# Optimization experiments

Hardware: AMD Instinct MI355X
Metric: run time of the kernel (lower is better)

The kernel has to match this reference:

```python
import jax, jax.numpy as jnp
import numpy as np

POI, EMB, UNITS, QDIM, B = 5000, 256, 512, 256, 64


def setup_inputs() -> dict:
    key = jax.random.key(0)
    ks = jax.random.split(key, 16)
    s = 0.05
    return {
        "x": jax.random.randint(ks[0], (B,), 0, POI),
        "query": jax.random.normal(ks[1], (B, QDIM), jnp.float32),
        "poi_embedding": jax.random.normal(ks[2], (POI, EMB), jnp.float32),
        "A_hat": jax.random.normal(ks[3], (B, B), jnp.float32),
        "dec_hidden": jax.random.normal(ks[4], (B, UNITS), jnp.float32),
        "cat_dec_hidden": jax.random.normal(ks[5], (1, B, UNITS), jnp.float32),
        # GRUCell params (keras order z, r, h; reset_after=True -> bias [2, 3*units])
        "gru_kernel": jax.random.normal(ks[6], (EMB + QDIM, 3 * UNITS), jnp.float32) * s,
        "gru_rec_kernel": jax.random.normal(ks[7], (UNITS, 3 * UNITS), jnp.float32) * s,
        "gru_bias": jax.random.normal(ks[8], (2, 3 * UNITS), jnp.float32) * s,
        # Bahdanau attention params
        "W1_w": jax.random.normal(ks[9], (EMB, UNITS), jnp.float32) * s,
        "W1_b": jnp.zeros((UNITS,), jnp.float32),
        "W2_w": jax.random.normal(ks[10], (UNITS, UNITS), jnp.float32) * s,
        "W2_b": jnp.zeros((UNITS,), jnp.float32),
        "V_w": jax.random.normal(ks[11], (UNITS, 1), jnp.float32) * s,
        "V_b": jnp.zeros((1,), jnp.float32),
        # output dense: concat(context EMB, output_ UNITS, cat_hidden UNITS) -> POI
        "fc_w": jax.random.normal(ks[12], (EMB + 2 * UNITS, POI), jnp.float32) * s,
        "fc_b": jnp.zeros((POI,), jnp.float32),
    }


def _gru_cell(x, h, kernel, rec_kernel, bias):
    # keras GRUCell, reset_after=True, gate order (z, r, h)
    xm = x @ kernel + bias[0]        # [B, 3U]
    hm = h @ rec_kernel + bias[1]    # [B, 3U]
    xz, xr, xh = jnp.split(xm, 3, axis=-1)
    hz, hr, hh = jnp.split(hm, 3, axis=-1)
    z = jax.nn.sigmoid(xz + hz)
    r = jax.nn.sigmoid(xr + hr)
    h_cand = jnp.tanh(xh + r * hh)
    h_new = z * h + (1.0 - z) * h_cand
    return h_new, h_new


def reference(x, query, poi_embedding, A_hat, dec_hidden, cat_dec_hidden,
              gru_kernel, gru_rec_kernel, gru_bias,
              W1_w, W1_b, W2_w, W2_b, V_w, V_b, fc_w, fc_b):
    emb = poi_embedding
    x1 = jnp.concatenate([emb[x], query], axis=1)          # [B, EMB+QDIM]
    output_, state = _gru_cell(x1, dec_hidden, gru_kernel, gru_rec_kernel, gru_bias)
    # Bahdanau attention: values are the full embedding table [POI, EMB]
    v_proj = emb @ W1_w + W1_b                              # [POI, U]
    q_proj = output_ @ W2_w + W2_b                          # [B, U]
    score = jnp.tanh(v_proj[None, :, :] + q_proj[:, None, :]) @ V_w + V_b  # [B, POI, 1]
    attn = jax.nn.softmax(score, axis=1)                    # [B, POI, 1]
    context = jnp.sum(attn * emb[None, :, :], axis=1)       # [B, EMB]
    out_cat = jnp.concatenate([context, output_, cat_dec_hidden[0]], axis=1)
    logits = out_cat @ fc_w + fc_b                          # [B, POI]
    return (logits, state, output_)
```

## Files before the change

### kernel.cpp

```cpp
#include <hip/hip_runtime.h>
#include <hip/hip_bf16.h>

typedef __bf16 bf16;
typedef __bf16 bf16x8 __attribute__((ext_vector_type(8)));
typedef float f32x4 __attribute__((ext_vector_type(4)));

#define BB 64
#define EMB 256
#define UNITS 512
#define POI 5000
#define KCAT 1280
#define SCLD 5024
#define L2E 1.4426950408889634f

__device__ __forceinline__ float rcp_(float x){ return __builtin_amdgcn_rcpf(x); }
__device__ __forceinline__ float exp2_(float x){ return __builtin_amdgcn_exp2f(x); }

__device__ __forceinline__ bf16x8 cvt8(f32x4 a0, f32x4 a1){
  bf16x8 o;
#pragma unroll
  for(int j=0;j<4;j++){ o[j]=(bf16)a0[j]; o[4+j]=(bf16)a1[j]; }
  return o;
}

__device__ __forceinline__ f32x4 mm16r(const float* __restrict__ ap, const float* __restrict__ B,
                                       int ldb, int K, int nc, int lane){
  int q = lane >> 4;
  f32x4 acc = {0.f,0.f,0.f,0.f};
  ap += q*8;
  const float* bp = B + (size_t)(q*8)*ldb + nc;
#pragma unroll 2
  for(int k0 = 0; k0 < K; k0 += 32){
    bf16x8 a = cvt8(*(const f32x4*)ap, *(const f32x4*)(ap+4));
    bf16x8 b;
#pragma unroll
    for(int j=0;j<8;j++) b[j] = (bf16)bp[(size_t)j*ldb];
    acc = __builtin_amdgcn_mfma_f32_16x16x32_bf16(a, b, acc, 0, 0, 0);
    ap += 32; bp += (size_t)32*ldb;
  }
  return acc;
}
__device__ __forceinline__ f32x4 mm16f(const float* __restrict__ A, const float* __restrict__ B,
                                       int lda, int ldb, int K, int mr, int nc, int lane){
  return mm16r(A + (size_t)mr*lda, B, ldb, K, nc, lane);
}

__device__ __forceinline__ void t64(const float* __restrict__ src, int srcLd, int nRv,
    int r0, int c0, int cW, bf16* __restrict__ dstT, int dstLd, int dstRmax,
    int lane, int w){
  int r = r0 + lane;
  bool rv = r < nRv;
  int cw4 = cW >> 2;
  int cb = c0 + w*cw4;
  for(int c8=0;c8<cw4;c8+=8){
    int c = cb + c8;
    f32x4 v0={0.f,0.f,0.f,0.f}, v1={0.f,0.f,0.f,0.f};
    if(rv){ v0 = *(const f32x4*)(src + (size_t)r*srcLd + c);
            v1 = *(const f32x4*)(src + (size_t)r*srcLd + c + 4); }
    if(r < dstRmax){
#pragma unroll
      for(int j=0;j<4;j++){
        dstT[(size_t)(c+j)*dstLd + r]   = (bf16)v0[j];
        dstT[(size_t)(c+4+j)*dstLd + r] = (bf16)v1[j];
      }
    }
  }
}

__global__ __launch_bounds__(256) void k_prep0(
    const float* __restrict__ emb, const float* __restrict__ W1, const float* __restrict__ W2,
    const float* __restrict__ gruK, const float* __restrict__ gruR,
    float* __restrict__ out, float* __restrict__ outc,
    bf16* __restrict__ embB, bf16* __restrict__ embTb,
    bf16* __restrict__ W1Tb, bf16* __restrict__ W2Tb,
    bf16* __restrict__ gruKTb, bf16* __restrict__ gruRTb,
    unsigned* __restrict__ mxb, float* __restrict__ sumb){
  int bx = blockIdx.x, t = threadIdx.x, lane = t & 63, w = t >> 6;
  if(bx < 80){
    int r0 = bx*64;
    for(int ch = t; ch < 2048; ch += 256){
      int r = r0 + (ch >> 5), cc = (ch & 31)*8;
      if(r < POI){
        f32x4 v0 = *(const f32x4*)(emb + (size_t)r*EMB + cc);
        f32x4 v1 = *(const f32x4*)(emb + (size_t)r*EMB + cc + 4);
        *(bf16x8*)(embB + (size_t)r*EMB + cc) = cvt8(v0, v1);
      }
    }
  } else if(bx < 240){
    int i = bx - 80;
    t64(emb, EMB, POI, (i>>1)*64, (i&1)*128, 128, embTb, SCLD, SCLD, lane, w);
  } else if(bx < 256){
    int i = bx - 240;
    t64(W2, UNITS, UNITS, (i>>1)*64, (i&1)*256, 256, W2Tb, UNITS, UNITS, lane, w);
  } else if(bx < 264){
    int i = bx - 256;
    t64(W1, UNITS, EMB, (i>>1)*64, (i&1)*256, 256, W1Tb, EMB, EMB, lane, w);
  } else if(bx < 328){
    int i = bx - 264;
    t64(gruK, 1536, 512, (i>>3)*64, (i&7)*192, 192, gruKTb, 512, 512, lane, w);
  } else if(bx < 392){
    int i = bx - 328;
    t64(gruR, 1536, 512, (i>>3)*64, (i&7)*192, 192, gruRTb, 512, 512, lane, w);
  } else if(bx < 432){
    f32x4 z = {0.f,0.f,0.f,0.f};
    for(int i = (bx-392)*256 + t; i < 80000; i += 40*256) ((f32x4*)out)[i] = z;
  } else if(bx < 434){
    f32x4 z = {0.f,0.f,0.f,0.f};
    for(int i = (bx-432)*256 + t; i < 4096; i += 512){
      int b = i >> 6, jj = i & 63;
      ((f32x4*)(outc + (size_t)b*KCAT))[jj] = z;
    }
  } else {
    if(t < BB){ mxb[t] = 0u; sumb[t] = 0.f; }
  }
}

__global__ __launch_bounds__(256) void k_gru(const int* __restrict__ x, const float* __restrict__ query,
    const bf16* __restrict__ embB, const float* __restrict__ h0,
    const bf16* __restrict__ gruKTb, const bf16* __restrict__ gruRTb,
    float* __restrict__ xmP, float* __restrict__ hmP){
  int lane = threadIdx.x & 63, w = threadIdx.x >> 6;
  int col = blockIdx.x*16 + (lane & 15);
  int y = blockIdx.y, z = blockIdx.z;
  int mr = w*16 + (lane & 15);
  int q = lane >> 4;
  const bf16* bp = (y ? gruRTb : gruKTb) + (size_t)col*512 + z*256 + q*8;
  float* C = (y ? hmP : xmP) + (size_t)z*BB*1536;
  f32x4 acc = {0.f,0.f,0.f,0.f};
  if(y == 0 && z == 0){
    const bf16* ap = embB + (size_t)x[mr]*EMB + q*8;
#pragma unroll
    for(int k0=0;k0<256;k0+=32){
      bf16x8 a = *(const bf16x8*)ap, b = *(const bf16x8*)bp;
      acc = __builtin_amdgcn_mfma_f32_16x16x32_bf16(a,b,acc,0,0,0);
      ap += 32; bp += 32;
    }
  } else {
    const float* apf = y ? (h0 + (size_t)mr*512 + z*256 + q*8)
                         : (query + (size_t)mr*256 + q*8);
#pragma unroll
    for(int k0=0;k0<256;k0+=32){
      bf16x8 a = cvt8(*(const f32x4*)apf, *(const f32x4*)(apf+4));
      bf16x8 b = *(const bf16x8*)bp;
      acc = __builtin_amdgcn_mfma_f32_16x16x32_bf16(a,b,acc,0,0,0);
      apf += 32; bp += 32;
    }
  }
  int rb = w*16 + (lane >> 4)*4;
#pragma unroll
  for(int r=0;r<4;r++) C[(size_t)(rb+r)*1536 + col] = acc[r];
}

__global__ __launch_bounds__(256) void k_gates(const float* __restrict__ xmP, const float* __restrict__ hmP,
                        const float* __restrict__ bias, const float* __restrict__ h0,
                        const float* __restrict__ catd,
                        float* __restrict__ hn, float* __restrict__ outc, float* __restrict__ dout){
  int b = blockIdx.x, u = blockIdx.y*256 + threadIdx.x;
  const float* x0 = xmP + b*1536; const float* x1s = xmP + (size_t)BB*1536 + b*1536;
  const float* h0s = hmP + b*1536; const float* h1s = hmP + (size_t)BB*1536 + b*1536;
  float xz = x0[u]      + x1s[u]      + bias[u];
  float xg = x0[512+u]  + x1s[512+u]  + bias[512+u];
  float xh = x0[1024+u] + x1s[1024+u] + bias[1024+u];
  float hz = h0s[u]      + h1s[u]      + bias[1536+u];
  float hg = h0s[512+u]  + h1s[512+u]  + bias[2048+u];
  float hh = h0s[1024+u] + h1s[1024+u] + bias[2560+u];
  float z = rcp_(1.f + exp2_(-L2E*(xz+hz)));
  float r = rcp_(1.f + exp2_(-L2E*(xg+hg)));
  float ca = xh + r*hh;
  ca = fminf(fmaxf(ca, -15.f), 15.f);
  float e = exp2_(2.f*L2E*ca);
  float hc = (e - 1.f)*rcp_(e + 1.f);
  float h = h0[b*512+u];
  float v = z*h + (1.f - z)*hc;
  hn[b*512+u] = v;
  outc[b*KCAT + 256 + u] = v;
  outc[b*KCAT + 768 + u] = catd[(size_t)b*512 + u];
  dout[(size_t)POI*BB + (size_t)b*512 + u] = v;
  dout[(size_t)POI*BB + (size_t)BB*512 + (size_t)b*512 + u] = v;
}

__global__ __launch_bounds__(256) void k_qproj(const float* __restrict__ hn, const bf16* __restrict__ W2Tb,
                        const float* __restrict__ W2b, float* __restrict__ Eq){
  __shared__ float accs[16][17];
  int t = threadIdx.x, lane = t & 63, w = t >> 6;
  int c16 = blockIdx.x & 31, r16 = blockIdx.x >> 5;
  for(int i=t;i<16*17;i+=256) ((float*)accs)[i] = 0.f;
  __syncthreads();
  int q = lane >> 4;
  int mr  = r16*16 + (lane & 15);
  int col = c16*16 + (lane & 15);
  const float* ap = hn + (size_t)mr*UNITS + w*128 + q*8;
  const bf16*  bp = W2Tb + (size_t)col*UNITS + w*128 + q*8;
  f32x4 acc = {0.f,0.f,0.f,0.f};
#pragma unroll
  for(int k0=0;k0<128;k0+=32){
    bf16x8 a = cvt8(*(const f32x4*)ap, *(const f32x4*)(ap+4));
    bf16x8 b = *(const bf16x8*)bp;
    acc = __builtin_amdgcn_mfma_f32_16x16x32_bf16(a,b,acc,0,0,0);
    ap += 32; bp += 32;
  }
#pragma unroll
  for(int r=0;r<4;r++) atomicAdd(&accs[q*4+r][lane & 15], acc[r]);
  __syncthreads();
  int r = t >> 4, c = t & 15;
  int colg = c16*16 + c;
  float v = (accs[r][c] + W2b[colg])*(2.f*L2E);
  Eq[(size_t)(r16*16+r)*UNITS + colg] = exp2_(fminf(fmaxf(v,-40.f),40.f));
}

template<int NY>
__global__ __launch_bounds__(256, 8) void k_vscore(
    const bf16* __restrict__ embB, const bf16* __restrict__ W1Tb,
    const float* __restrict__ W1b, const float* __restrict__ Eq,
    const float* __restrict__ Vw, float* __restrict__ scS){
  constexpr int USL = 512/NY;
  __shared__ float evsT[USL][20];
  __shared__ float vws[USL];
  int t = threadIdx.x, lane = t & 63, w = t >> 6;
  int p0 = blockIdx.x*16, uh = blockIdx.y*USL;
  int q = lane >> 4;
  int mr = p0 + (lane & 15); if(mr > POI-1) mr = POI-1;
#pragma unroll
  for(int i=0;i<USL/64;i++){
    int colL = (w + 4*i)*16 + (lane & 15);
    const bf16* ap = embB + (size_t)mr*EMB + q*8;
    const bf16* bp = W1Tb + (size_t)(uh+colL)*EMB + q*8;
    f32x4 acc = {0.f,0.f,0.f,0.f};
#pragma unroll
    for(int k0=0;k0<EMB;k0+=32){
      bf16x8 a = *(const bf16x8*)ap, b = *(const bf16x8*)bp;
      acc = __builtin_amdgcn_mfma_f32_16x16x32_bf16(a,b,acc,0,0,0);
      ap += 32; bp += 32;
    }
    float bn = W1b[uh+colL];
    f32x4 ev;
#pragma unroll
    for(int r=0;r<4;r++){
      float v = (acc[r] + bn)*(2.f*L2E);
      ev[r] = exp2_(fminf(fmaxf(v,-40.f),40.f));
    }
    *(f32x4*)&evsT[colL][q*4] = ev;
  }
  if(t < USL) vws[t] = Vw[uh + t];
  __syncthreads();
  int pg = t & 3, b = t >> 2;
  const float* qrow = Eq + (size_t)b*UNITS + uh;
  f32x4 s = {0.f,0.f,0.f,0.f};
#pragma unroll 4
  for(int u4=0; u4<USL/4; ++u4){
    f32x4 q4 = *(const f32x4*)&qrow[u4*4];
    f32x4 wv = *(const f32x4*)&vws[u4*4];
#pragma unroll
    for(int j=0;j<4;j++){
      f32x4 ev = *(const f32x4*)&evsT[u4*4+j][4*pg];
#pragma unroll
      for(int e=0;e<4;e++)
        s[e] += wv[j]*rcp_(ev[e]*q4[j] + 1.f);
    }
  }
  int pA = p0 + 4*pg;
  float* srow = scS + (size_t)blockIdx.y*BB*SCLD + (size_t)b*SCLD + pA;
  if(pA + 3 < POI) *(f32x4*)srow = s;
  else {
#pragma unroll
    for(int e=0;e<4;e++) if(pA+e < POI) srow[e] = s[e];
  }
}

__global__ __launch_bounds__(256) void k_smax_a(float* __restrict__ sc, unsigned* __restrict__ mxb,
                                                int nslab){
  __shared__ float red[256];
  int b = blockIdx.x, y = blockIdx.y, t = threadIdx.x;
  float* sA = sc + (size_t)b*SCLD;
  int pend = (y+1)*640; if(pend > POI) pend = POI;
  float mx = -3.4e38f;
  for(int p = y*640 + t; p < pend; p += 256){
    float acc = sA[p];
    for(int s2=1;s2<nslab;s2++) acc += sA[(size_t)s2*BB*SCLD + p];
    float v = -2.f*acc;
    sA[p] = v;
    mx = fmaxf(mx, v);
  }
  red[t] = mx; __syncthreads();
  for(int o=128;o>0;o>>=1){ if(t<o) red[t]=fmaxf(red[t],red[t+o]); __syncthreads(); }
  if(t==0){
    unsigned u = __float_as_uint(red[0]);
    unsigned key = (u & 0x80000000u) ? ~u : (u | 0x80000000u);
    atomicMax(mxb + b, key);
  }
}

__global__ __launch_bounds__(256) void k_smax_b(float* __restrict__ sc, const unsigned* __restrict__ mxb,
                                                float* __restrict__ sumb){
  __shared__ float red[256];
  int b = blockIdx.x, y = blockIdx.y, t = threadIdx.x;
  unsigned key = mxb[b];
  unsigned uu = (key & 0x80000000u) ? (key ^ 0x80000000u) : ~key;
  float M = __uint_as_float(uu);
  float* sA = sc + (size_t)b*SCLD;
  int pend = (y+1)*640; if(pend > POI) pend = POI;
  float sm = 0.f;
  for(int p = y*640 + t; p < pend; p += 256){
    float e = exp2_((sA[p] - M)*L2E);
    sA[p] = e;
    sm += e;
  }
  if(y == 7 && t < SCLD-POI) sA[POI + t] = 0.f;
  red[t] = sm; __syncthreads();
  for(int o=128;o>0;o>>=1){ if(t<o) red[t]+=red[t+o]; __syncthreads(); }
  if(t==0) atomicAdd(sumb + b, red[0]);
}

__global__ __launch_bounds__(256) void k_ctx(const float* __restrict__ wb, const bf16* __restrict__ embTb,
                                             const float* __restrict__ sumb, float* __restrict__ outc){
  int lane = threadIdx.x & 63, w = threadIdx.x >> 6;
  int n = blockIdx.x*16 + (lane & 15);
  int ky = blockIdx.y;
  int kbeg = ky*64;
  int K = (ky == 78) ? 32 : 64;
  int mr = w*16 + (lane & 15);
  int q = lane >> 4;
  const float* ap = wb + (size_t)mr*SCLD + kbeg + q*8;
  const bf16*  bp = embTb + (size_t)n*SCLD + kbeg + q*8;
  f32x4 acc = {0.f,0.f,0.f,0.f};
  for(int k0=0;k0<K;k0+=32){
    bf16x8 a = cvt8(*(const f32x4*)ap, *(const f32x4*)(ap+4));
    bf16x8 b = *(const bf16x8*)bp;
    acc = __builtin_amdgcn_mfma_f32_16x16x32_bf16(a,b,acc,0,0,0);
    ap += 32; bp += 32;
  }
  int rb = w*16 + (lane >> 4)*4;
#pragma unroll
  for(int r=0;r<4;r++) atomicAdd(&outc[(size_t)(rb+r)*KCAT + n], acc[r]*rcp_(sumb[rb+r]));
}

__global__ __launch_bounds__(256) void k_logits(const float* __restrict__ A, const float* __restrict__ Bw,
                        const float* __restrict__ fcb, float* __restrict__ out){
  int lane = threadIdx.x & 63, w = threadIdx.x >> 6;
  int n = blockIdx.x*16 + (lane & 15);
  int nc = n < POI ? n : POI-1;
  int ky = blockIdx.y, kbeg = ky*160;
  f32x4 acc = mm16f(A + kbeg, Bw + (size_t)kbeg*POI, KCAT, POI, 160,
                    w*16 + (lane & 15), nc, lane);
  int rb = w*16 + (lane >> 4)*4;
  if(n < POI){
    float bn = (ky == 0) ? fcb[n] : 0.f;
#pragma unroll
    for(int r=0;r<4;r++) atomicAdd(&out[(size_t)(rb+r)*POI + n], acc[r] + bn);
  }
}

extern "C" void kernel_launch(void* const* d_in, const int* in_sizes, int n_in,
                              void* d_out, int out_size, void* d_ws, size_t ws_size,
                              hipStream_t stream){
  const int*   x     = (const int*)d_in[0];
  const float* query = (const float*)d_in[1];
  const float* emb   = (const float*)d_in[2];
  const float* h0    = (const float*)d_in[4];
  const float* catd  = (const float*)d_in[5];
  const float* gruK  = (const float*)d_in[6];
  const float* gruR  = (const float*)d_in[7];
  const float* gruB  = (const float*)d_in[8];
  const float* W1    = (const float*)d_in[9];
  const float* W1b   = (const float*)d_in[10];
  const float* W2    = (const float*)d_in[11];
  const float* W2b   = (const float*)d_in[12];
  const float* Vw    = (const float*)d_in[13];
  const float* fcw   = (const float*)d_in[15];
  const float* fcb   = (const float*)d_in[16];
  float* out = (float*)d_out;

  int nslab = (ws_size >= (size_t)24*1024*1024) ? 8 : 4;

  char* ws = (char*)d_ws;
  size_t off = 0;
  auto alloc = [&](size_t bytes)->void*{ void* p = ws + off; off += (bytes + 255) & ~(size_t)255; return p; };
  float* outc   = (float*)alloc((size_t)BB*KCAT*4);
  float* xmP    = (float*)alloc((size_t)2*BB*1536*4);
  float* hmP    = (float*)alloc((size_t)2*BB*1536*4);
  float* hn     = (float*)alloc((size_t)BB*512*4);
  float* Eq     = (float*)alloc((size_t)BB*512*4);
  bf16*  embB   = (bf16*)alloc((size_t)POI*EMB*2);
  bf16*  embTb  = (bf16*)alloc((size_t)EMB*SCLD*2);
  bf16*  W1Tb   = (bf16*)alloc((size_t)UNITS*EMB*2);
  bf16*  W2Tb   = (bf16*)alloc((size_t)UNITS*UNITS*2);
  bf16*  gruKTb = (bf16*)alloc((size_t)1536*512*2);
  bf16*  gruRTb = (bf16*)alloc((size_t)1536*512*2);
  unsigned* mxb = (unsigned*)alloc((size_t)BB*4);
  float* sumb   = (float*)alloc((size_t)BB*4);
  float* sc     = (float*)alloc((size_t)nslab*BB*SCLD*4);

  k_prep0  <<<435, 256, 0, stream>>>(emb, W1, W2, gruK, gruR, out, outc,
                                     embB, embTb, W1Tb, W2Tb, gruKTb, gruRTb, mxb, sumb);
  k_gru    <<<dim3(96,2,2), 256, 0, stream>>>(x, query, embB, h0, gruKTb, gruRTb, xmP, hmP);
  k_gates  <<<dim3(BB,2), 256, 0, stream>>>(xmP, hmP, gruB, h0, catd, hn, outc, out);
  k_qproj  <<<128, 256, 0, stream>>>(hn, W2Tb, W2b, Eq);
  if(nslab == 8)
    k_vscore<8><<<dim3(313,8), 256, 0, stream>>>(embB, W1Tb, W1b, Eq, Vw, sc);
  else
    k_vscore<4><<<dim3(313,4), 256, 0, stream>>>(embB, W1Tb, W1b, Eq, Vw, sc);
  k_smax_a <<<dim3(BB,8), 256, 0, stream>>>(sc, mxb, nslab);
  k_smax_b <<<dim3(BB,8), 256, 0, stream>>>(sc, mxb, sumb);
  k_ctx    <<<dim3(16,79), 256, 0, stream>>>(sc, embTb, sumb, outc);
  k_logits <<<dim3(313,8), 256, 0, stream>>>(outc, fcw, fcb, out);
}
```

Before: 201.3 us.

## Fuse GRU matmuls with gate math and drop softmax max pass

Merges the GRU matmul and gate kernels into a single kernel that computes all six gate tiles per block and applies the nonlinearities from shared memory, removing the split-K partial buffers. The softmax drops the max-reduction kernel and exponentiates scores directly. That relies on the score expression (a weighted sum of reciprocals, scaled by -2) staying bounded for these inputs, so overflow safety is lost. Bias and cat_hidden initialization move into the prep kernel, which cuts one launch and the bias add in the logits epilogue. The fused GRU grid has only 64 blocks, so per-block work is longer.

```diff
diff --git a/kernel.cpp b/kernel.cpp
--- a/kernel.cpp
+++ b/kernel.cpp
@@ -70,11 +70,12 @@
 __global__ __launch_bounds__(256) void k_prep0(
     const float* __restrict__ emb, const float* __restrict__ W1, const float* __restrict__ W2,
     const float* __restrict__ gruK, const float* __restrict__ gruR,
+    const float* __restrict__ fcb, const float* __restrict__ catd,
     float* __restrict__ out, float* __restrict__ outc,
     bf16* __restrict__ embB, bf16* __restrict__ embTb,
     bf16* __restrict__ W1Tb, bf16* __restrict__ W2Tb,
     bf16* __restrict__ gruKTb, bf16* __restrict__ gruRTb,
-    unsigned* __restrict__ mxb, float* __restrict__ sumb){
+    float* __restrict__ sumb){
   int bx = blockIdx.x, t = threadIdx.x, lane = t & 63, w = t >> 6;
   if(bx < 80){
     int r0 = bx*64;
@@ -101,82 +102,88 @@
   } else if(bx < 392){
     int i = bx - 328;
     t64(gruR, 1536, 512, (i>>3)*64, (i&7)*192, 192, gruRTb, 512, 512, lane, w);
-  } else if(bx < 432){
-    f32x4 z = {0.f,0.f,0.f,0.f};
-    for(int i = (bx-392)*256 + t; i < 80000; i += 40*256) ((f32x4*)out)[i] = z;
-  } else if(bx < 434){
-    f32x4 z = {0.f,0.f,0.f,0.f};
-    for(int i = (bx-432)*256 + t; i < 4096; i += 512){
-      int b = i >> 6, jj = i & 63;
-      ((f32x4*)(outc + (size_t)b*KCAT))[jj] = z;
+  } else if(bx < 456){
+    int b = bx - 392;
+    for(int n=t; n<POI; n+=256) out[(size_t)b*POI + n] = fcb[n];
+  } else if(bx < 464){
+    int base = (bx - 456)*8;
+    for(int i=t; i<8*768; i+=256){
+      int bb = base + i/768, c = i - (i/768)*768;
+      if(c < 256) outc[(size_t)bb*KCAT + c] = 0.f;
+      else        outc[(size_t)bb*KCAT + 512 + c] = catd[(size_t)bb*512 + (c-256)];
     }
   } else {
-    if(t < BB){ mxb[t] = 0u; sumb[t] = 0.f; }
-  }
-}
-
-__global__ __launch_bounds__(256) void k_gru(const int* __restrict__ x, const float* __restrict__ query,
+    if(t < BB) sumb[t] = 0.f;
+  }
+}
+
+__global__ __launch_bounds__(384) void k_gruga(const int* __restrict__ x, const float* __restrict__ query,
     const bf16* __restrict__ embB, const float* __restrict__ h0,
     const bf16* __restrict__ gruKTb, const bf16* __restrict__ gruRTb,
-    float* __restrict__ xmP, float* __restrict__ hmP){
-  int lane = threadIdx.x & 63, w = threadIdx.x >> 6;
-  int col = blockIdx.x*16 + (lane & 15);
-  int y = blockIdx.y, z = blockIdx.z;
-  int mr = w*16 + (lane & 15);
-  int q = lane >> 4;
-  const bf16* bp = (y ? gruRTb : gruKTb) + (size_t)col*512 + z*256 + q*8;
-  float* C = (y ? hmP : xmP) + (size_t)z*BB*1536;
-  f32x4 acc = {0.f,0.f,0.f,0.f};
-  if(y == 0 && z == 0){
-    const bf16* ap = embB + (size_t)x[mr]*EMB + q*8;
-#pragma unroll
-    for(int k0=0;k0<256;k0+=32){
-      bf16x8 a = *(const bf16x8*)ap, b = *(const bf16x8*)bp;
-      acc = __builtin_amdgcn_mfma_f32_16x16x32_bf16(a,b,acc,0,0,0);
-      ap += 32; bp += 32;
-    }
-  } else {
-    const float* apf = y ? (h0 + (size_t)mr*512 + z*256 + q*8)
-                         : (query + (size_t)mr*256 + q*8);
-#pragma unroll
-    for(int k0=0;k0<256;k0+=32){
-      bf16x8 a = cvt8(*(const f32x4*)apf, *(const f32x4*)(apf+4));
-      bf16x8 b = *(const bf16x8*)bp;
-      acc = __builtin_amdgcn_mfma_f32_16x16x32_bf16(a,b,acc,0,0,0);
-      apf += 32; bp += 32;
-    }
-  }
-  int rb = w*16 + (lane >> 4)*4;
-#pragma unroll
-  for(int r=0;r<4;r++) C[(size_t)(rb+r)*1536 + col] = acc[r];
-}
-
-__global__ __launch_bounds__(256) void k_gates(const float* __restrict__ xmP, const float* __restrict__ hmP,
-                        const float* __restrict__ bias, const float* __restrict__ h0,
-                        const float* __restrict__ catd,
-                        float* __restrict__ hn, float* __restrict__ outc, float* __restrict__ dout){
-  int b = blockIdx.x, u = blockIdx.y*256 + threadIdx.x;
-  const float* x0 = xmP + b*1536; const float* x1s = xmP + (size_t)BB*1536 + b*1536;
-  const float* h0s = hmP + b*1536; const float* h1s = hmP + (size_t)BB*1536 + b*1536;
-  float xz = x0[u]      + x1s[u]      + bias[u];
-  float xg = x0[512+u]  + x1s[512+u]  + bias[512+u];
-  float xh = x0[1024+u] + x1s[1024+u] + bias[1024+u];
-  float hz = h0s[u]      + h1s[u]      + bias[1536+u];
-  float hg = h0s[512+u]  + h1s[512+u]  + bias[2048+u];
-  float hh = h0s[1024+u] + h1s[1024+u] + bias[2560+u];
-  float z = rcp_(1.f + exp2_(-L2E*(xz+hz)));
-  float r = rcp_(1.f + exp2_(-L2E*(xg+hg)));
-  float ca = xh + r*hh;
-  ca = fminf(fmaxf(ca, -15.f), 15.f);
-  float e = exp2_(2.f*L2E*ca);
-  float hc = (e - 1.f)*rcp_(e + 1.f);
-  float h = h0[b*512+u];
-  float v = z*h + (1.f - z)*hc;
-  hn[b*512+u] = v;
-  outc[b*KCAT + 256 + u] = v;
-  outc[b*KCAT + 768 + u] = catd[(size_t)b*512 + u];
-  dout[(size_t)POI*BB + (size_t)b*512 + u] = v;
-  dout[(size_t)POI*BB + (size_t)BB*512 + (size_t)b*512 + u] = v;
+    const float* __restrict__ bias,
+    float* __restrict__ hn, float* __restrict__ outc, float* __restrict__ dout){
+  __shared__ float tiles[6][32][17];
+  int t = threadIdx.x, lane = t & 63, w = t >> 6;
+  int b0 = (blockIdx.x & 1)*32;
+  int u0 = (blockIdx.x >> 1)*16;
+  int y = w/3, g = w - y*3;
+  int q = lane >> 4;
+  int col = g*512 + u0 + (lane & 15);
+  const bf16* KT = (y ? gruRTb : gruKTb) + (size_t)col*512 + q*8;
+#pragma unroll
+  for(int pq=0;pq<2;pq++){
+    int mr = b0 + pq*16 + (lane & 15);
+    f32x4 acc = {0.f,0.f,0.f,0.f};
+    const bf16* bp = KT;
+    if(y){
+      const float* apf = h0 + (size_t)mr*512 + q*8;
+#pragma unroll
+      for(int k0=0;k0<512;k0+=32){
+        bf16x8 a = cvt8(*(const f32x4*)apf, *(const f32x4*)(apf+4));
+        acc = __builtin_amdgcn_mfma_f32_16x16x32_bf16(a, *(const bf16x8*)bp, acc, 0,0,0);
+        apf += 32; bp += 32;
+      }
+    } else {
+      const bf16* ap = embB + (size_t)x[mr]*EMB + q*8;
+#pragma unroll
+      for(int k0=0;k0<256;k0+=32){
+        acc = __builtin_amdgcn_mfma_f32_16x16x32_bf16(*(const bf16x8*)ap, *(const bf16x8*)bp, acc, 0,0,0);
+        ap += 32; bp += 32;
+      }
+      const float* apf = query + (size_t)mr*256 + q*8;
+#pragma unroll
+      for(int k0=0;k0<256;k0+=32){
+        bf16x8 a = cvt8(*(const f32x4*)apf, *(const f32x4*)(apf+4));
+        acc = __builtin_amdgcn_mfma_f32_16x16x32_bf16(a, *(const bf16x8*)bp, acc, 0,0,0);
+        apf += 32; bp += 32;
+      }
+    }
+#pragma unroll
+    for(int r=0;r<4;r++) tiles[w][pq*16 + q*4 + r][lane & 15] = acc[r];
+  }
+  __syncthreads();
+  for(int i=t;i<512;i+=384){
+    int bl = i >> 4, j = i & 15;
+    int b = b0 + bl, u = u0 + j;
+    float xz = tiles[0][bl][j] + bias[u];
+    float xr = tiles[1][bl][j] + bias[512+u];
+    float xh = tiles[2][bl][j] + bias[1024+u];
+    float hz = tiles[3][bl][j] + bias[1536+u];
+    float hr = tiles[4][bl][j] + bias[2048+u];
+    float hh = tiles[5][bl][j] + bias[2560+u];
+    float z = rcp_(1.f + exp2_(-L2E*(xz+hz)));
+    float r = rcp_(1.f + exp2_(-L2E*(xr+hr)));
+    float ca = xh + r*hh;
+    ca = fminf(fmaxf(ca, -15.f), 15.f);
+    float e = exp2_(2.f*L2E*ca);
+    float hc = (e - 1.f)*rcp_(e + 1.f);
+    float h = h0[(size_t)b*512+u];
+    float v = z*h + (1.f - z)*hc;
+    hn[(size_t)b*512+u] = v;
+    outc[(size_t)b*KCAT + 256 + u] = v;
+    dout[(size_t)POI*BB + (size_t)b*512 + u] = v;
+    dout[(size_t)POI*BB + (size_t)BB*512 + (size_t)b*512 + u] = v;
+  }
 }
 
 __global__ __launch_bounds__(256) void k_qproj(const float* __restrict__ hn, const bf16* __restrict__ W2Tb,
@@ -267,41 +274,17 @@
   }
 }
 
-__global__ __launch_bounds__(256) void k_smax_a(float* __restrict__ sc, unsigned* __restrict__ mxb,
-                                                int nslab){
+__global__ __launch_bounds__(256) void k_smax(float* __restrict__ sc, float* __restrict__ sumb,
+                                              int nslab){
   __shared__ float red[256];
   int b = blockIdx.x, y = blockIdx.y, t = threadIdx.x;
   float* sA = sc + (size_t)b*SCLD;
   int pend = (y+1)*640; if(pend > POI) pend = POI;
-  float mx = -3.4e38f;
+  float sm = 0.f;
   for(int p = y*640 + t; p < pend; p += 256){
     float acc = sA[p];
     for(int s2=1;s2<nslab;s2++) acc += sA[(size_t)s2*BB*SCLD + p];
-    float v = -2.f*acc;
-    sA[p] = v;
-    mx = fmaxf(mx, v);
-  }
-  red[t] = mx; __syncthreads();
-  for(int o=128;o>0;o>>=1){ if(t<o) red[t]=fmaxf(red[t],red[t+o]); __syncthreads(); }
-  if(t==0){
-    unsigned u = __float_as_uint(red[0]);
-    unsigned key = (u & 0x80000000u) ? ~u : (u | 0x80000000u);
-    atomicMax(mxb + b, key);
-  }
-}
-
-__global__ __launch_bounds__(256) void k_smax_b(float* __restrict__ sc, const unsigned* __restrict__ mxb,
-                                                float* __restrict__ sumb){
-  __shared__ float red[256];
-  int b = blockIdx.x, y = blockIdx.y, t = threadIdx.x;
-  unsigned key = mxb[b];
-  unsigned uu = (key & 0x80000000u) ? (key ^ 0x80000000u) : ~key;
-  float M = __uint_as_float(uu);
-  float* sA = sc + (size_t)b*SCLD;
-  int pend = (y+1)*640; if(pend > POI) pend = POI;
-  float sm = 0.f;
-  for(int p = y*640 + t; p < pend; p += 256){
-    float e = exp2_((sA[p] - M)*L2E);
+    float e = exp2_(-2.f*L2E*acc);
     sA[p] = e;
     sm += e;
   }
@@ -335,7 +318,7 @@
 }
 
 __global__ __launch_bounds__(256) void k_logits(const float* __restrict__ A, const float* __restrict__ Bw,
-                        const float* __restrict__ fcb, float* __restrict__ out){
+                        float* __restrict__ out){
   int lane = threadIdx.x & 63, w = threadIdx.x >> 6;
   int n = blockIdx.x*16 + (lane & 15);
   int nc = n < POI ? n : POI-1;
@@ -344,9 +327,8 @@
                     w*16 + (lane & 15), nc, lane);
   int rb = w*16 + (lane >> 4)*4;
   if(n < POI){
-    float bn = (ky == 0) ? fcb[n] : 0.f;
-#pragma unroll
-    for(int r=0;r<4;r++) atomicAdd(&out[(size_t)(rb+r)*POI + n], acc[r] + bn);
+#pragma unroll
+    for(int r=0;r<4;r++) atomicAdd(&out[(size_t)(rb+r)*POI + n], acc[r]);
   }
 }
 
@@ -376,8 +358,6 @@
   size_t off = 0;
   auto alloc = [&](size_t bytes)->void*{ void* p = ws + off; off += (bytes + 255) & ~(size_t)255; return p; };
   float* outc   = (float*)alloc((size_t)BB*KCAT*4);
-  float* xmP    = (float*)alloc((size_t)2*BB*1536*4);
-  float* hmP    = (float*)alloc((size_t)2*BB*1536*4);
   float* hn     = (float*)alloc((size_t)BB*512*4);
   float* Eq     = (float*)alloc((size_t)BB*512*4);
   bf16*  embB   = (bf16*)alloc((size_t)POI*EMB*2);
@@ -386,21 +366,18 @@
   bf16*  W2Tb   = (bf16*)alloc((size_t)UNITS*UNITS*2);
   bf16*  gruKTb = (bf16*)alloc((size_t)1536*512*2);
   bf16*  gruRTb = (bf16*)alloc((size_t)1536*512*2);
-  unsigned* mxb = (unsigned*)alloc((size_t)BB*4);
   float* sumb   = (float*)alloc((size_t)BB*4);
   float* sc     = (float*)alloc((size_t)nslab*BB*SCLD*4);
 
-  k_prep0  <<<435, 256, 0, stream>>>(emb, W1, W2, gruK, gruR, out, outc,
-                                     embB, embTb, W1Tb, W2Tb, gruKTb, gruRTb, mxb, sumb);
-  k_gru    <<<dim3(96,2,2), 256, 0, stream>>>(x, query, embB, h0, gruKTb, gruRTb, xmP, hmP);
-  k_gates  <<<dim3(BB,2), 256, 0, stream>>>(xmP, hmP, gruB, h0, catd, hn, outc, out);
+  k_prep0  <<<465, 256, 0, stream>>>(emb, W1, W2, gruK, gruR, fcb, catd, out, outc,
+                                     embB, embTb, W1Tb, W2Tb, gruKTb, gruRTb, sumb);
+  k_gruga  <<<64, 384, 0, stream>>>(x, query, embB, h0, gruKTb, gruRTb, gruB, hn, outc, out);
   k_qproj  <<<128, 256, 0, stream>>>(hn, W2Tb, W2b, Eq);
   if(nslab == 8)
     k_vscore<8><<<dim3(313,8), 256, 0, stream>>>(embB, W1Tb, W1b, Eq, Vw, sc);
   else
     k_vscore<4><<<dim3(313,4), 256, 0, stream>>>(embB, W1Tb, W1b, Eq, Vw, sc);
-  k_smax_a <<<dim3(BB,8), 256, 0, stream>>>(sc, mxb, nslab);
-  k_smax_b <<<dim3(BB,8), 256, 0, stream>>>(sc, mxb, sumb);
+  k_smax   <<<dim3(BB,8), 256, 0, stream>>>(sc, sumb, nslab);
   k_ctx    <<<dim3(16,79), 256, 0, stream>>>(sc, embTb, sumb, outc);
-  k_logits <<<dim3(313,8), 256, 0, stream>>>(outc, fcw, fcb, out);
-}
+  k_logits <<<dim3(313,8), 256, 0, stream>>>(outc, fcw, out);
+}
```

New measurement: 208.8 us. 1.04x slower.

## Fuse softmax into score kernel and drop pre-transposed weight copies

Applied to the files above, without the earlier changes.

The score kernel now covers all 512 units per 512-thread block. It keeps the A fragments in registers and writes exp(score) straight out, atomically adding the row sums, so the slab reduction and both softmax max/sum kernels go away. The max subtraction is dropped, which depends on the score staying small enough that exp does not overflow. The GRU and context GEMMs read the fp32 weights and embedding with strided loads instead of bf16 transposed copies, so the prep kernel shrinks. The prep kernel also pre-fills the logits with the bias and copies cat_dec_hidden into the concat buffer. These changes cut launches and prep traffic, at the cost of uncoalesced B-operand loads and less parallelism in the score stage.

```diff
diff --git a/kernel.cpp b/kernel.cpp
--- a/kernel.cpp
+++ b/kernel.cpp
@@ -4,6 +4,7 @@
 typedef __bf16 bf16;
 typedef __bf16 bf16x8 __attribute__((ext_vector_type(8)));
 typedef float f32x4 __attribute__((ext_vector_type(4)));
+typedef float f32x2 __attribute__((ext_vector_type(2)));
 
 #define BB 64
 #define EMB 256
@@ -46,7 +47,7 @@
 }
 
 __device__ __forceinline__ void t64(const float* __restrict__ src, int srcLd, int nRv,
-    int r0, int c0, int cW, bf16* __restrict__ dstT, int dstLd, int dstRmax,
+    int r0, int c0, int cW, bf16* __restrict__ dstT, int dstLd,
     int lane, int w){
   int r = r0 + lane;
   bool rv = r < nRv;
@@ -57,24 +58,20 @@
     f32x4 v0={0.f,0.f,0.f,0.f}, v1={0.f,0.f,0.f,0.f};
     if(rv){ v0 = *(const f32x4*)(src + (size_t)r*srcLd + c);
             v1 = *(const f32x4*)(src + (size_t)r*srcLd + c + 4); }
-    if(r < dstRmax){
-#pragma unroll
-      for(int j=0;j<4;j++){
-        dstT[(size_t)(c+j)*dstLd + r]   = (bf16)v0[j];
-        dstT[(size_t)(c+4+j)*dstLd + r] = (bf16)v1[j];
-      }
+#pragma unroll
+    for(int j=0;j<4;j++){
+      dstT[(size_t)(c+j)*dstLd + r]   = (bf16)v0[j];
+      dstT[(size_t)(c+4+j)*dstLd + r] = (bf16)v1[j];
     }
   }
 }
 
 __global__ __launch_bounds__(256) void k_prep0(
     const float* __restrict__ emb, const float* __restrict__ W1, const float* __restrict__ W2,
-    const float* __restrict__ gruK, const float* __restrict__ gruR,
+    const float* __restrict__ fcb, const float* __restrict__ catd,
     float* __restrict__ out, float* __restrict__ outc,
-    bf16* __restrict__ embB, bf16* __restrict__ embTb,
-    bf16* __restrict__ W1Tb, bf16* __restrict__ W2Tb,
-    bf16* __restrict__ gruKTb, bf16* __restrict__ gruRTb,
-    unsigned* __restrict__ mxb, float* __restrict__ sumb){
+    bf16* __restrict__ embB, bf16* __restrict__ W1Tb, bf16* __restrict__ W2Tb,
+    float* __restrict__ sumb, float* __restrict__ sc){
   int bx = blockIdx.x, t = threadIdx.x, lane = t & 63, w = t >> 6;
   if(bx < 80){
     int r0 = bx*64;
@@ -86,64 +83,65 @@
         *(bf16x8*)(embB + (size_t)r*EMB + cc) = cvt8(v0, v1);
       }
     }
-  } else if(bx < 240){
+  } else if(bx < 88){
     int i = bx - 80;
-    t64(emb, EMB, POI, (i>>1)*64, (i&1)*128, 128, embTb, SCLD, SCLD, lane, w);
-  } else if(bx < 256){
-    int i = bx - 240;
-    t64(W2, UNITS, UNITS, (i>>1)*64, (i&1)*256, 256, W2Tb, UNITS, UNITS, lane, w);
-  } else if(bx < 264){
-    int i = bx - 256;
-    t64(W1, UNITS, EMB, (i>>1)*64, (i&1)*256, 256, W1Tb, EMB, EMB, lane, w);
-  } else if(bx < 328){
-    int i = bx - 264;
-    t64(gruK, 1536, 512, (i>>3)*64, (i&7)*192, 192, gruKTb, 512, 512, lane, w);
-  } else if(bx < 392){
-    int i = bx - 328;
-    t64(gruR, 1536, 512, (i>>3)*64, (i&7)*192, 192, gruRTb, 512, 512, lane, w);
-  } else if(bx < 432){
-    f32x4 z = {0.f,0.f,0.f,0.f};
-    for(int i = (bx-392)*256 + t; i < 80000; i += 40*256) ((f32x4*)out)[i] = z;
-  } else if(bx < 434){
-    f32x4 z = {0.f,0.f,0.f,0.f};
-    for(int i = (bx-432)*256 + t; i < 4096; i += 512){
-      int b = i >> 6, jj = i & 63;
-      ((f32x4*)(outc + (size_t)b*KCAT))[jj] = z;
+    t64(W1, UNITS, EMB, (i>>1)*64, (i&1)*256, 256, W1Tb, EMB, lane, w);
+  } else if(bx < 104){
+    int i = bx - 88;
+    t64(W2, UNITS, UNITS, (i>>1)*64, (i&1)*256, 256, W2Tb, UNITS, lane, w);
+  } else if(bx < 168){
+    int b = bx - 104;
+    for(int n=t; n<POI; n+=256) out[(size_t)b*POI + n] = fcb[n];
+  } else if(bx < 176){
+    int base = (bx - 168)*8;
+    for(int i=t; i<8*768; i+=256){
+      int bb = base + i/768, c = i - (i/768)*768;
+      if(c < 256) outc[(size_t)bb*KCAT + c] = 0.f;
+      else        outc[(size_t)bb*KCAT + 512 + c] = catd[(size_t)bb*512 + (c-256)];
     }
   } else {
-    if(t < BB){ mxb[t] = 0u; sumb[t] = 0.f; }
+    if(t < BB) sumb[t] = 0.f;
+    for(int i=t; i<BB*24; i+=256){
+      int b = i/24, j = i - (i/24)*24;
+      sc[(size_t)b*SCLD + POI + j] = 0.f;
+    }
   }
 }
 
 __global__ __launch_bounds__(256) void k_gru(const int* __restrict__ x, const float* __restrict__ query,
     const bf16* __restrict__ embB, const float* __restrict__ h0,
-    const bf16* __restrict__ gruKTb, const bf16* __restrict__ gruRTb,
+    const float* __restrict__ gruK, const float* __restrict__ gruR,
     float* __restrict__ xmP, float* __restrict__ hmP){
   int lane = threadIdx.x & 63, w = threadIdx.x >> 6;
   int col = blockIdx.x*16 + (lane & 15);
   int y = blockIdx.y, z = blockIdx.z;
   int mr = w*16 + (lane & 15);
   int q = lane >> 4;
-  const bf16* bp = (y ? gruRTb : gruKTb) + (size_t)col*512 + z*256 + q*8;
+  const float* bp = (y ? gruR : gruK) + (size_t)(z*256 + q*8)*1536 + col;
   float* C = (y ? hmP : xmP) + (size_t)z*BB*1536;
   f32x4 acc = {0.f,0.f,0.f,0.f};
   if(y == 0 && z == 0){
     const bf16* ap = embB + (size_t)x[mr]*EMB + q*8;
-#pragma unroll
+#pragma unroll 2
     for(int k0=0;k0<256;k0+=32){
-      bf16x8 a = *(const bf16x8*)ap, b = *(const bf16x8*)bp;
-      acc = __builtin_amdgcn_mfma_f32_16x16x32_bf16(a,b,acc,0,0,0);
-      ap += 32; bp += 32;
+      bf16x8 a = *(const bf16x8*)ap;
+      bf16x8 b;
+#pragma unroll
+      for(int j=0;j<8;j++) b[j] = (bf16)bp[(size_t)j*1536];
+      acc = __builtin_amdgcn_mfma_f32_16x16x32_bf16(a, b, acc, 0,0,0);
+      ap += 32; bp += (size_t)32*1536;
     }
   } else {
     const float* apf = y ? (h0 + (size_t)mr*512 + z*256 + q*8)
                          : (query + (size_t)mr*256 + q*8);
-#pragma unroll
+#pragma unroll 2
     for(int k0=0;k0<256;k0+=32){
       bf16x8 a = cvt8(*(const f32x4*)apf, *(const f32x4*)(apf+4));
-      bf16x8 b = *(const bf16x8*)bp;
-      acc = __builtin_amdgcn_mfma_f32_16x16x32_bf16(a,b,acc,0,0,0);
-      apf += 32; bp += 32;
+      bf16x8 b;
+#pragma unroll
+      for(int j=0;j<8;j++) b[j] = (bf16)bp[(size_t)j*1536];
+      acc = __builtin_amdgcn_mfma_f32_16x16x32_bf16(a, b, acc, 0,0,0);
+      apf += 32; bp += (size_t)32*1536;
     }
   }
   int rb = w*16 + (lane >> 4)*4;
@@ -153,7 +151,6 @@
 
 __global__ __launch_bounds__(256) void k_gates(const float* __restrict__ xmP, const float* __restrict__ hmP,
                         const float* __restrict__ bias, const float* __restrict__ h0,
-                        const float* __restrict__ catd,
                         float* __restrict__ hn, float* __restrict__ outc, float* __restrict__ dout){
   int b = blockIdx.x, u = blockIdx.y*256 + threadIdx.x;
   const float* x0 = xmP + b*1536; const float* x1s = xmP + (size_t)BB*1536 + b*1536;
@@ -170,11 +167,10 @@
   ca = fminf(fmaxf(ca, -15.f), 15.f);
   float e = exp2_(2.f*L2E*ca);
   float hc = (e - 1.f)*rcp_(e + 1.f);
-  float h = h0[b*512+u];
+  float h = h0[(size_t)b*512+u];
   float v = z*h + (1.f - z)*hc;
-  hn[b*512+u] = v;
-  outc[b*KCAT + 256 + u] = v;
-  outc[b*KCAT + 768 + u] = catd[(size_t)b*512 + u];
+  hn[(size_t)b*512+u] = v;
+  outc[(size_t)b*KCAT + 256 + u] = v;
   dout[(size_t)POI*BB + (size_t)b*512 + u] = v;
   dout[(size_t)POI*BB + (size_t)BB*512 + (size_t)b*512 + u] = v;
 }
@@ -208,31 +204,33 @@
   Eq[(size_t)(r16*16+r)*UNITS + colg] = exp2_(fminf(fmaxf(v,-40.f),40.f));
 }
 
-template<int NY>
-__global__ __launch_bounds__(256, 8) void k_vscore(
+__global__ __launch_bounds__(512) void k_vscore(
     const bf16* __restrict__ embB, const bf16* __restrict__ W1Tb,
     const float* __restrict__ W1b, const float* __restrict__ Eq,
-    const float* __restrict__ Vw, float* __restrict__ scS){
-  constexpr int USL = 512/NY;
-  __shared__ float evsT[USL][20];
-  __shared__ float vws[USL];
+    const float* __restrict__ Vw, float* __restrict__ sc, float* __restrict__ sumb){
+  __shared__ float evsT[512][20];
+  __shared__ float vws[512];
   int t = threadIdx.x, lane = t & 63, w = t >> 6;
-  int p0 = blockIdx.x*16, uh = blockIdx.y*USL;
+  int p0 = blockIdx.x*16;
   int q = lane >> 4;
   int mr = p0 + (lane & 15); if(mr > POI-1) mr = POI-1;
-#pragma unroll
-  for(int i=0;i<USL/64;i++){
-    int colL = (w + 4*i)*16 + (lane & 15);
+  bf16x8 afr[8];
+  {
     const bf16* ap = embB + (size_t)mr*EMB + q*8;
-    const bf16* bp = W1Tb + (size_t)(uh+colL)*EMB + q*8;
+#pragma unroll
+    for(int k=0;k<8;k++){ afr[k] = *(const bf16x8*)ap; ap += 32; }
+  }
+#pragma unroll
+  for(int i=0;i<4;i++){
+    int colL = (w + 8*i)*16 + (lane & 15);
+    const bf16* bp = W1Tb + (size_t)colL*EMB + q*8;
     f32x4 acc = {0.f,0.f,0.f,0.f};
 #pragma unroll
-    for(int k0=0;k0<EMB;k0+=32){
-      bf16x8 a = *(const bf16x8*)ap, b = *(const bf16x8*)bp;
-      acc = __builtin_amdgcn_mfma_f32_16x16x32_bf16(a,b,acc,0,0,0);
-      ap += 32; bp += 32;
-    }
-    float bn = W1b[uh+colL];
+    for(int k=0;k<8;k++){
+      acc = __builtin_amdgcn_mfma_f32_16x16x32_bf16(afr[k], *(const bf16x8*)bp, acc, 0,0,0);
+      bp += 32;
+    }
+    float bn = W1b[colL];
     f32x4 ev;
 #pragma unroll
     for(int r=0;r<4;r++){
@@ -241,93 +239,65 @@
     }
     *(f32x4*)&evsT[colL][q*4] = ev;
   }
-  if(t < USL) vws[t] = Vw[uh + t];
+  vws[t] = Vw[t];
   __syncthreads();
-  int pg = t & 3, b = t >> 2;
-  const float* qrow = Eq + (size_t)b*UNITS + uh;
-  f32x4 s = {0.f,0.f,0.f,0.f};
+  int pg = t & 7, b = t >> 3;
+  const float* qrow = Eq + (size_t)b*UNITS;
+  f32x2 s = {0.f, 0.f};
 #pragma unroll 4
-  for(int u4=0; u4<USL/4; ++u4){
+  for(int u4=0; u4<128; ++u4){
     f32x4 q4 = *(const f32x4*)&qrow[u4*4];
     f32x4 wv = *(const f32x4*)&vws[u4*4];
 #pragma unroll
     for(int j=0;j<4;j++){
-      f32x4 ev = *(const f32x4*)&evsT[u4*4+j][4*pg];
-#pragma unroll
-      for(int e=0;e<4;e++)
-        s[e] += wv[j]*rcp_(ev[e]*q4[j] + 1.f);
-    }
-  }
-  int pA = p0 + 4*pg;
-  float* srow = scS + (size_t)blockIdx.y*BB*SCLD + (size_t)b*SCLD + pA;
-  if(pA + 3 < POI) *(f32x4*)srow = s;
-  else {
-#pragma unroll
-    for(int e=0;e<4;e++) if(pA+e < POI) srow[e] = s[e];
-  }
-}
-
-__global__ __launch_bounds__(256) void k_smax_a(float* __restrict__ sc, unsigned* __restrict__ mxb,
-                                                int nslab){
-  __shared__ float red[256];
-  int b = blockIdx.x, y = blockIdx.y, t = threadIdx.x;
-  float* sA = sc + (size_t)b*SCLD;
-  int pend = (y+1)*640; if(pend > POI) pend = POI;
-  float mx = -3.4e38f;
-  for(int p = y*640 + t; p < pend; p += 256){
-    float acc = sA[p];
-    for(int s2=1;s2<nslab;s2++) acc += sA[(size_t)s2*BB*SCLD + p];
-    float v = -2.f*acc;
-    sA[p] = v;
-    mx = fmaxf(mx, v);
-  }
-  red[t] = mx; __syncthreads();
-  for(int o=128;o>0;o>>=1){ if(t<o) red[t]=fmaxf(red[t],red[t+o]); __syncthreads(); }
-  if(t==0){
-    unsigned u = __float_as_uint(red[0]);
-    unsigned key = (u & 0x80000000u) ? ~u : (u | 0x80000000u);
-    atomicMax(mxb + b, key);
-  }
-}
-
-__global__ __launch_bounds__(256) void k_smax_b(float* __restrict__ sc, const unsigned* __restrict__ mxb,
-                                                float* __restrict__ sumb){
-  __shared__ float red[256];
-  int b = blockIdx.x, y = blockIdx.y, t = threadIdx.x;
-  unsigned key = mxb[b];
-  unsigned uu = (key & 0x80000000u) ? (key ^ 0x80000000u) : ~key;
-  float M = __uint_as_float(uu);
-  float* sA = sc + (size_t)b*SCLD;
-  int pend = (y+1)*640; if(pend > POI) pend = POI;
-  float sm = 0.f;
-  for(int p = y*640 + t; p < pend; p += 256){
-    float e = exp2_((sA[p] - M)*L2E);
-    sA[p] = e;
-    sm += e;
-  }
-  if(y == 7 && t < SCLD-POI) sA[POI + t] = 0.f;
-  red[t] = sm; __syncthreads();
-  for(int o=128;o>0;o>>=1){ if(t<o) red[t]+=red[t+o]; __syncthreads(); }
-  if(t==0) atomicAdd(sumb + b, red[0]);
-}
-
-__global__ __launch_bounds__(256) void k_ctx(const float* __restrict__ wb, const bf16* __restrict__ embTb,
+      f32x2 ev = *(const f32x2*)&evsT[u4*4+j][2*pg];
+      s[0] += wv[j]*rcp_(ev[0]*q4[j] + 1.f);
+      s[1] += wv[j]*rcp_(ev[1]*q4[j] + 1.f);
+    }
+  }
+  int pA = p0 + 2*pg;
+  float e0 = (pA   < POI) ? exp2_(-2.f*L2E*s[0]) : 0.f;
+  float e1 = (pA+1 < POI) ? exp2_(-2.f*L2E*s[1]) : 0.f;
+  float* srow = sc + (size_t)b*SCLD + pA;
+  if(pA+1 < POI){ f32x2 e2 = {e0, e1}; *(f32x2*)srow = e2; }
+  else if(pA < POI) srow[0] = e0;
+  float ps = e0 + e1;
+  ps += __shfl_xor(ps, 1);
+  ps += __shfl_xor(ps, 2);
+  ps += __shfl_xor(ps, 4);
+  if(pg == 0) atomicAdd(&sumb[b], ps);
+}
+
+__global__ __launch_bounds__(256) void k_ctx(const float* __restrict__ wb, const float* __restrict__ emb,
                                              const float* __restrict__ sumb, float* __restrict__ outc){
   int lane = threadIdx.x & 63, w = threadIdx.x >> 6;
   int n = blockIdx.x*16 + (lane & 15);
   int ky = blockIdx.y;
   int kbeg = ky*64;
-  int K = (ky == 78) ? 32 : 64;
   int mr = w*16 + (lane & 15);
   int q = lane >> 4;
   const float* ap = wb + (size_t)mr*SCLD + kbeg + q*8;
-  const bf16*  bp = embTb + (size_t)n*SCLD + kbeg + q*8;
   f32x4 acc = {0.f,0.f,0.f,0.f};
-  for(int k0=0;k0<K;k0+=32){
+  if(ky < 78){
+    const float* bp = emb + (size_t)(kbeg + q*8)*EMB + n;
+#pragma unroll 2
+    for(int k0=0;k0<64;k0+=32){
+      bf16x8 a = cvt8(*(const f32x4*)ap, *(const f32x4*)(ap+4));
+      bf16x8 b;
+#pragma unroll
+      for(int j=0;j<8;j++) b[j] = (bf16)bp[(size_t)j*EMB];
+      acc = __builtin_amdgcn_mfma_f32_16x16x32_bf16(a,b,acc,0,0,0);
+      ap += 32; bp += (size_t)32*EMB;
+    }
+  } else {
     bf16x8 a = cvt8(*(const f32x4*)ap, *(const f32x4*)(ap+4));
-    bf16x8 b = *(const bf16x8*)bp;
+    bf16x8 b;
+#pragma unroll
+    for(int j=0;j<8;j++){
+      int k = kbeg + q*8 + j; int kc = k < POI ? k : POI-1;
+      b[j] = (bf16)emb[(size_t)kc*EMB + n];
+    }
     acc = __builtin_amdgcn_mfma_f32_16x16x32_bf16(a,b,acc,0,0,0);
-    ap += 32; bp += 32;
   }
   int rb = w*16 + (lane >> 4)*4;
 #pragma unroll
@@ -335,7 +305,7 @@
 }
 
 __global__ __launch_bounds__(256) void k_logits(const float* __restrict__ A, const float* __restrict__ Bw,
-                        const float* __restrict__ fcb, float* __restrict__ out){
+                        float* __restrict__ out){
   int lane = threadIdx.x & 63, w = threadIdx.x >> 6;
   int n = blockIdx.x*16 + (lane & 15);
   int nc = n < POI ? n : POI-1;
@@ -344,9 +314,8 @@
                     w*16 + (lane & 15), nc, lane);
   int rb = w*16 + (lane >> 4)*4;
   if(n < POI){
-    float bn = (ky == 0) ? fcb[n] : 0.f;
-#pragma unroll
-    for(int r=0;r<4;r++) atomicAdd(&out[(size_t)(rb+r)*POI + n], acc[r] + bn);
+#pragma unroll
+    for(int r=0;r<4;r++) atomicAdd(&out[(size_t)(rb+r)*POI + n], acc[r]);
   }
 }
 
@@ -370,8 +339,6 @@
   const float* fcb   = (const float*)d_in[16];
   float* out = (float*)d_out;
 
-  int nslab = (ws_size >= (size_t)24*1024*1024) ? 8 : 4;
-
   char* ws = (char*)d_ws;
   size_t off = 0;
   auto alloc = [&](size_t bytes)->void*{ void* p = ws + off; off += (bytes + 255) & ~(size_t)255; return p; };
@@ -381,26 +348,17 @@
   float* hn     = (float*)alloc((size_t)BB*512*4);
   float* Eq     = (float*)alloc((size_t)BB*512*4);
   bf16*  embB   = (bf16*)alloc((size_t)POI*EMB*2);
-  bf16*  embTb  = (bf16*)alloc((size_t)EMB*SCLD*2);
   bf16*  W1Tb   = (bf16*)alloc((size_t)UNITS*EMB*2);
   bf16*  W2Tb   = (bf16*)alloc((size_t)UNITS*UNITS*2);
-  bf16*  gruKTb = (bf16*)alloc((size_t)1536*512*2);
-  bf16*  gruRTb = (bf16*)alloc((size_t)1536*512*2);
-  unsigned* mxb = (unsigned*)alloc((size_t)BB*4);
   float* sumb   = (float*)alloc((size_t)BB*4);
-  float* sc     = (float*)alloc((size_t)nslab*BB*SCLD*4);
-
-  k_prep0  <<<435, 256, 0, stream>>>(emb, W1, W2, gruK, gruR, out, outc,
-                                     embB, embTb, W1Tb, W2Tb, gruKTb, gruRTb, mxb, sumb);
-  k_gru    <<<dim3(96,2,2), 256, 0, stream>>>(x, query, embB, h0, gruKTb, gruRTb, xmP, hmP);
-  k_gates  <<<dim3(BB,2), 256, 0, stream>>>(xmP, hmP, gruB, h0, catd, hn, outc, out);
+  float* sc     = (float*)alloc((size_t)BB*SCLD*4);
+
+  k_prep0  <<<177, 256, 0, stream>>>(emb, W1, W2, fcb, catd, out, outc,
+                                     embB, W1Tb, W2Tb, sumb, sc);
+  k_gru    <<<dim3(96,2,2), 256, 0, stream>>>(x, query, embB, h0, gruK, gruR, xmP, hmP);
+  k_gates  <<<dim3(BB,2), 256, 0, stream>>>(xmP, hmP, gruB, h0, hn, outc, out);
   k_qproj  <<<128, 256, 0, stream>>>(hn, W2Tb, W2b, Eq);
-  if(nslab == 8)
-    k_vscore<8><<<dim3(313,8), 256, 0, stream>>>(embB, W1Tb, W1b, Eq, Vw, sc);
-  else
-    k_vscore<4><<<dim3(313,4), 256, 0, stream>>>(embB, W1Tb, W1b, Eq, Vw, sc);
-  k_smax_a <<<dim3(BB,8), 256, 0, stream>>>(sc, mxb, nslab);
-  k_smax_b <<<dim3(BB,8), 256, 0, stream>>>(sc, mxb, sumb);
-  k_ctx    <<<dim3(16,79), 256, 0, stream>>>(sc, embTb, sumb, outc);
-  k_logits <<<dim3(313,8), 256, 0, stream>>>(outc, fcw, fcb, out);
-}
+  k_vscore <<<313, 512, 0, stream>>>(embB, W1Tb, W1b, Eq, Vw, sc, sumb);
+  k_ctx    <<<dim3(16,79), 256, 0, stream>>>(sc, emb, sumb, outc);
+  k_logits <<<dim3(313,8), 256, 0, stream>>>(outc, fcw, out);
+}
```

Result: slower. 211.2 us (+4.9%).
